# Kernel optimization log

Hardware: AMD Instinct MI355X
Metric: run time of the kernel (lower is better)

## Reference

```python
import jax, jax.numpy as jnp
import numpy as np

T, A = 2048, 64          # n_thread, n_agents
RAWOB, N_TP, N_GP = 120, 5, 2
E = N_TP * N_GP          # number of sub-nets (type x group placeholder)
D = RAWOB + N_TP + 1     # augmented obs dim fed to each Net
H = 128                  # hidden width of each sub-net MLP
N_ACTION = 16


def setup_inputs() -> dict:
    key = jax.random.key(0)
    ks = jax.random.split(key, 12)
    s1 = 1.0 / np.sqrt(D)
    s2 = 1.0 / np.sqrt(H)
    return {
        "obs": jax.random.normal(ks[0], (T, A, RAWOB), dtype=jnp.float32),
        "hete_pick": jax.random.randint(ks[1], (T, A), 0, E),
        "hete_type": jax.random.randint(ks[2], (T, A), 0, N_TP),
        "gp_sel_summary": jax.random.randint(ks[3], (T, N_TP), 0, N_GP),
        # per-expert actor MLP params [E, ...]
        "W1": jax.random.normal(ks[4], (E, D, H), dtype=jnp.float32) * s1,
        "b1": jnp.zeros((E, H), dtype=jnp.float32),
        "W2": jax.random.normal(ks[5], (E, H, N_ACTION), dtype=jnp.float32) * s2,
        "b2": jnp.zeros((E, N_ACTION), dtype=jnp.float32),
        # central critic params
        "Wc1": jax.random.normal(ks[6], (D, H), dtype=jnp.float32) * s1,
        "bc1": jnp.zeros((H,), dtype=jnp.float32),
        "Wc2": jax.random.normal(ks[7], (H, 1), dtype=jnp.float32) * s2,
        "bc2": jnp.zeros((1,), dtype=jnp.float32),
    }


def _augment_obs(obs, hete_type, gp_sel_summary):
    # obs <- cat(obs, hete_type, gp_sel_summary with -1 scattered at own type idx)
    t, a, _ = obs.shape
    n_tp = gp_sel_summary.shape[1]
    gp = jnp.broadcast_to(gp_sel_summary[:, None, :].astype(obs.dtype), (t, a, n_tp))
    oh = jax.nn.one_hot(hete_type, n_tp, dtype=obs.dtype)
    gp_obs = gp * (1.0 - oh) - oh  # scatter -1 at index hete_type
    return jnp.concatenate([obs, hete_type[..., None].astype(obs.dtype), gp_obs], axis=-1)


def reference(obs, hete_pick, hete_type, gp_sel_summary,
              W1, b1, W2, b2, Wc1, bc1, Wc2, bc2):
    t, a, _ = obs.shape
    x = _augment_obs(obs, hete_type, gp_sel_summary)          # [T, A, D]
    xf = x.reshape(t * a, -1)                                  # [N, D]
    pick = hete_pick.reshape(t * a)                            # [N]
    n_exp = W1.shape[0]
    # dispatch: each token routed to exactly one sub-net; dense compute + masked combine
    logits = jnp.zeros((t * a, W2.shape[-1]), dtype=obs.dtype)
    for e in range(n_exp):  # small fixed expert loop
        y = jax.nn.relu(xf @ W1[e] + b1[e]) @ W2[e] + b2[e]    # [N, n_action]
        logits = jnp.where((pick == e)[:, None], y, logits)
    logits = logits.reshape(t, a, -1)
    # central critic on all tokens
    value = (jax.nn.relu(xf @ Wc1 + bc1) @ Wc2 + bc2).reshape(t, a, 1)
    return logits, value
```

## Files before the change

kernel.cpp:

```cpp
#include <hip/hip_runtime.h>
#include <hip/hip_bf16.h>

#define T_DIM   2048
#define A_DIM   64
#define N_TOK   (T_DIM * A_DIM)
#define RAWOB   120
#define N_TP    5
#define E_EXP   10
#define D_DIM   126
#define DP      128
#define H_DIM   128
#define N_ACT   16
#define CAP     14336
#define BTOK    256
#define MAXC    (CAP / BTOK)
#define LOGITS_SZ (N_TOK * N_ACT)
#define HB_STRIDE 136

typedef __bf16 bh8 __attribute__((ext_vector_type(8)));
typedef ushort u16x8 __attribute__((ext_vector_type(8)));
typedef float  f32x4 __attribute__((ext_vector_type(4)));

__device__ __forceinline__ f32x4 mfma16(bh8 a, bh8 b, f32x4 c) {
    return __builtin_amdgcn_mfma_f32_16x16x32_bf16(a, b, c, 0, 0, 0);
}

__device__ __forceinline__ ushort f2bf(float f) {
    unsigned x = __builtin_bit_cast(unsigned, f);
    unsigned r = (x + 0x7fffu + ((x >> 16) & 1u)) >> 16;
    return (ushort)r;
}

#define W1P_N (E_EXP * H_DIM * DP)
#define W2P_N (E_EXP * N_ACT * H_DIM)
#define WC1P_N (DP * DP)

#define PB_BLOCKS 252

__global__ __launch_bounds__(256) void prep_bucket_kernel(
    const float* __restrict__ W1, const float* __restrict__ W2,
    const float* __restrict__ Wc1, const int* __restrict__ pick,
    int* __restrict__ counts, int* __restrict__ order,
    ushort* __restrict__ W1p, ushort* __restrict__ W2p, ushort* __restrict__ Wc1p)
{
    int bx = blockIdx.x, tid = threadIdx.x;
    if (bx < 44) {
        __shared__ ushort st[32][130];
        const float* src;
        ushort* dstbase;
        int kt;
        if (bx < 40) {
            int e = bx >> 2;
            kt = bx & 3;
            src = W1 + (e * D_DIM + kt * 32) * H_DIM;
            dstbase = W1p + e * (H_DIM * DP);
        } else {
            kt = bx - 40;
            src = Wc1 + kt * 32 * H_DIM;
            dstbase = Wc1p;
        }
        int dmax = D_DIM - kt * 32;
#pragma unroll
        for (int p = 0; p < 16; ++p) {
            int idx = p * 256 + tid;
            int dd = idx >> 7, n = idx & 127;
            float v = (dd < dmax) ? src[dd * H_DIM + n] : 0.f;
            st[dd][n] = f2bf(v);
        }
        __syncthreads();
#pragma unroll
        for (int p = 0; p < 16; ++p) {
            int idx = p * 256 + tid;
            int dd = idx >> 7, n = idx & 127;
            dstbase[((n >> 4) * 4 + kt) * 512 + ((dd >> 3) * 16 + (n & 15)) * 8 + (dd & 7)]
                = st[dd][n];
        }
    } else if (bx < 124) {
        int i = (bx - 44) * 256 + tid;
        int j = i & 7;
        int l = (i >> 3) & 63;
        int kt = (i >> 9) & 3;
        int e = i >> 11;
        int lm = l & 15, lq = l >> 4;
        W2p[i] = f2bf(W2[(e * H_DIM + kt * 32 + lq * 8 + j) * N_ACT + lm]);
    } else {
        __shared__ int lc[E_EXP], lb[E_EXP], lcur[E_EXP];
        if (tid < E_EXP) { lc[tid] = 0; lcur[tid] = 0; }
        __syncthreads();
        int base = (bx - 124) * 1024;
        int e4[4];
#pragma unroll
        for (int it = 0; it < 4; ++it) {
            e4[it] = pick[base + it * 256 + tid];
            atomicAdd(&lc[e4[it]], 1);
        }
        __syncthreads();
        if (tid < E_EXP) lb[tid] = atomicAdd(&counts[tid * 16], lc[tid]);
        __syncthreads();
#pragma unroll
        for (int it = 0; it < 4; ++it) {
            int e = e4[it];
            int pos = lb[e] + atomicAdd(&lcur[e], 1);
            if (pos < CAP) order[e * CAP + pos] = base + it * 256 + tid;
        }
    }
}

__global__ __launch_bounds__(512, 4) void moe_kernel(
    const float* __restrict__ obs, const int* __restrict__ hete_type,
    const int* __restrict__ gp_sel,
    const float* __restrict__ b1, const float* __restrict__ b2,
    const float* __restrict__ bc1, const float* __restrict__ bc2,
    const int* __restrict__ counts, const int* __restrict__ order,
    const ushort* __restrict__ W1p, const ushort* __restrict__ W2p,
    const ushort* __restrict__ Wc1p, const float* __restrict__ Wc2,
    float* __restrict__ out)
{
    __shared__ __align__(16) ushort wlds[18432];
    __shared__ __align__(16) ushort hbuf[8][16 * HB_STRIDE];

    const int bx = blockIdx.x;
    const int e = bx % E_EXP;
    const int c = bx / E_EXP;
    const int cnt = counts[e * 16];
    const int start = c * BTOK;
    if (start >= cnt) return;

    const int tid = threadIdx.x;
    const int w = tid >> 6;
    const int base = start + w * 32;
    const int l = tid & 63;
    const int lm = l & 15;
    const int lq = l >> 4;

    {
        const u16x8* s1 = (const u16x8*)(const void*)(W1p + e * (H_DIM * DP));
        u16x8* d1 = (u16x8*)(void*)wlds;
#pragma unroll
        for (int p = 0; p < 4; ++p) d1[p * 512 + tid] = s1[p * 512 + tid];
        if (tid < 256)
            ((u16x8*)(void*)(wlds + 16384))[tid] =
                ((const u16x8*)(const void*)(W2p + e * 2048))[tid];
    }

    const int* ord_e = order + e * CAP;

    bh8 a[2][4];
#pragma unroll
    for (int mt = 0; mt < 2; ++mt) {
        const int slot = min(base + mt * 16 + lm, cnt - 1);
        const int tok = ord_e[slot];
        const float* orow = obs + tok * RAWOB;
#pragma unroll
        for (int kt = 0; kt < 3; ++kt) {
            const float* p = orow + kt * 32 + lq * 8;
            float4 u0 = *(const float4*)(const void*)p;
            float4 u1 = *(const float4*)(const void*)(p + 4);
            u16x8 t;
            t[0] = f2bf(u0.x); t[1] = f2bf(u0.y); t[2] = f2bf(u0.z); t[3] = f2bf(u0.w);
            t[4] = f2bf(u1.x); t[5] = f2bf(u1.y); t[6] = f2bf(u1.z); t[7] = f2bf(u1.w);
            a[mt][kt] = __builtin_bit_cast(bh8, t);
        }
        u16x8 t;
        if (lq < 3) {
            const float* p = orow + 96 + lq * 8;
            float4 u0 = *(const float4*)(const void*)p;
            float4 u1 = *(const float4*)(const void*)(p + 4);
            t[0] = f2bf(u0.x); t[1] = f2bf(u0.y); t[2] = f2bf(u0.z); t[3] = f2bf(u0.w);
            t[4] = f2bf(u1.x); t[5] = f2bf(u1.y); t[6] = f2bf(u1.z); t[7] = f2bf(u1.w);
        } else {
            int ht = hete_type[tok];
            int tt = tok >> 6;
            t[0] = f2bf((float)ht);
#pragma unroll
            for (int q = 0; q < N_TP; ++q) {
                float g = (q == ht) ? -1.0f : (float)gp_sel[tt * N_TP + q];
                t[1 + q] = f2bf(g);
            }
            t[6] = 0; t[7] = 0;
        }
        a[mt][3] = __builtin_bit_cast(bh8, t);
    }

    float bnv[8];
#pragma unroll
    for (int nt = 0; nt < 8; ++nt) bnv[nt] = b1[e * H_DIM + nt * 16 + lm];
    const float bb  = b2[e * N_ACT + lm];
    const float bcv = bc2[0];

    __syncthreads();

    ushort* hrow = &hbuf[w][0];
#pragma unroll
    for (int mt = 0; mt < 2; ++mt) {
#pragma unroll
        for (int nt = 0; nt < 8; ++nt) {
            const int n = nt * 16 + lm;
            f32x4 ae = (f32x4){0.f, 0.f, 0.f, 0.f};
#pragma unroll
            for (int kt = 0; kt < 4; ++kt) {
                bh8 be = *(const bh8*)(const void*)(wlds + (nt * 4 + kt) * 512 + l * 8);
                ae = mfma16(a[mt][kt], be, ae);
            }
            float bn = bnv[nt];
#pragma unroll
            for (int r = 0; r < 4; ++r)
                hrow[(lq * 4 + r) * HB_STRIDE + n] = f2bf(fmaxf(ae[r] + bn, 0.f));
        }
        f32x4 y = (f32x4){0.f, 0.f, 0.f, 0.f};
#pragma unroll
        for (int kt = 0; kt < 4; ++kt) {
            bh8 bf = *(const bh8*)(const void*)(wlds + 16384 + kt * 512 + l * 8);
            bh8 hf = *(const bh8*)(const void*)(hrow + lm * HB_STRIDE + kt * 32 + lq * 8);
            y = mfma16(hf, bf, y);
        }
#pragma unroll
        for (int r = 0; r < 4; ++r) {
            int m = mt * 16 + lq * 4 + r;
            if (base + m < cnt)
                out[ord_e[base + m] * N_ACT + lm] = y[r] + bb;
        }
    }

    __syncthreads();

    {
        const u16x8* s1 = (const u16x8*)(const void*)Wc1p;
        u16x8* d1 = (u16x8*)(void*)wlds;
#pragma unroll
        for (int p = 0; p < 4; ++p) d1[p * 512 + tid] = s1[p * 512 + tid];
    }
    __syncthreads();

    {
        float part[2][4] = {{0.f,0.f,0.f,0.f},{0.f,0.f,0.f,0.f}};
#pragma unroll
        for (int nt = 0; nt < 8; ++nt) {
            const int n = nt * 16 + lm;
            f32x4 ac0 = (f32x4){0.f,0.f,0.f,0.f}, ac1 = ac0;
#pragma unroll
            for (int kt = 0; kt < 4; ++kt) {
                bh8 bc = *(const bh8*)(const void*)(wlds + (nt * 4 + kt) * 512 + l * 8);
                ac0 = mfma16(a[0][kt], bc, ac0);
                ac1 = mfma16(a[1][kt], bc, ac1);
            }
            float cn = bc1[n], wc = Wc2[n];
#pragma unroll
            for (int r = 0; r < 4; ++r) {
                part[0][r] += fmaxf(ac0[r] + cn, 0.f) * wc;
                part[1][r] += fmaxf(ac1[r] + cn, 0.f) * wc;
            }
        }
#pragma unroll
        for (int mask = 1; mask < 16; mask <<= 1)
#pragma unroll
            for (int mt = 0; mt < 2; ++mt)
#pragma unroll
                for (int r = 0; r < 4; ++r)
                    part[mt][r] += __shfl_xor(part[mt][r], mask, 64);
        if (lm == 0) {
#pragma unroll
            for (int mt = 0; mt < 2; ++mt)
#pragma unroll
                for (int r = 0; r < 4; ++r) {
                    int m = mt * 16 + lq * 4 + r;
                    if (base + m < cnt)
                        out[LOGITS_SZ + ord_e[base + m]] = part[mt][r] + bcv;
                }
        }
    }
}

extern "C" void kernel_launch(void* const* d_in, const int* in_sizes, int n_in,
                              void* d_out, int out_size, void* d_ws, size_t ws_size,
                              hipStream_t stream) {
    const float* obs  = (const float*)d_in[0];
    const int*   pick = (const int*)d_in[1];
    const int*   htyp = (const int*)d_in[2];
    const int*   gp   = (const int*)d_in[3];
    const float* W1   = (const float*)d_in[4];
    const float* b1   = (const float*)d_in[5];
    const float* W2   = (const float*)d_in[6];
    const float* b2   = (const float*)d_in[7];
    const float* Wc1  = (const float*)d_in[8];
    const float* bc1  = (const float*)d_in[9];
    const float* Wc2  = (const float*)d_in[10];
    const float* bc2  = (const float*)d_in[11];
    float* out = (float*)d_out;

    int*    counts = (int*)d_ws;
    int*    order  = counts + 160;
    ushort* W1p    = (ushort*)(order + E_EXP * CAP);
    ushort* W2p    = W1p + W1P_N;
    ushort* Wc1p   = W2p + W2P_N;

    hipMemsetAsync(counts, 0, 160 * sizeof(int), stream);
    prep_bucket_kernel<<<PB_BLOCKS, 256, 0, stream>>>(
        W1, W2, Wc1, pick, counts, order, W1p, W2p, Wc1p);
    moe_kernel<<<E_EXP * MAXC, 512, 0, stream>>>(
        obs, htyp, gp, b1, b2, bc1, bc2, counts, order,
        W1p, W2p, Wc1p, Wc2, out);
}
```

Measured before the change: 139.6 us.

## Keep MLP hidden in registers via transposed MFMA and fold biases into weights

The first-layer MFMA now runs with swapped operands (weights as A, activations as B), so the hidden activations come out in a layout that feeds straight into a K=16 bf16 MFMA for the second layer. This removes the per-wave LDS hidden buffer and its write/read round trip. Biases b1/bc1 are folded into the packed weight matrix as an extra K row, matched by a constant 1.0 input column, so the bias adds go away. The critic reduction becomes a lane-local dot product plus two shuffles instead of a 16-lane butterfly. Dropping the hidden buffer frees LDS, and launch bounds go up to 8 waves-per-EU occupancy, which may add register pressure.

```diff
diff --git a/kernel.cpp b/kernel.cpp
--- a/kernel.cpp
+++ b/kernel.cpp
@@ -15,14 +15,18 @@
 #define BTOK    256
 #define MAXC    (CAP / BTOK)
 #define LOGITS_SZ (N_TOK * N_ACT)
-#define HB_STRIDE 136
 
 typedef __bf16 bh8 __attribute__((ext_vector_type(8)));
 typedef ushort u16x8 __attribute__((ext_vector_type(8)));
+typedef ushort u16x4 __attribute__((ext_vector_type(4)));
+typedef short  s16x4 __attribute__((ext_vector_type(4)));
 typedef float  f32x4 __attribute__((ext_vector_type(4)));
 
 __device__ __forceinline__ f32x4 mfma16(bh8 a, bh8 b, f32x4 c) {
     return __builtin_amdgcn_mfma_f32_16x16x32_bf16(a, b, c, 0, 0, 0);
+}
+__device__ __forceinline__ f32x4 mfma16k16(s16x4 a, s16x4 b, f32x4 c) {
+    return __builtin_amdgcn_mfma_f32_16x16x16bf16_1k(a, b, c, 0, 0, 0);
 }
 
 __device__ __forceinline__ ushort f2bf(float f) {
@@ -39,7 +43,8 @@
 
 __global__ __launch_bounds__(256) void prep_bucket_kernel(
     const float* __restrict__ W1, const float* __restrict__ W2,
-    const float* __restrict__ Wc1, const int* __restrict__ pick,
+    const float* __restrict__ Wc1, const float* __restrict__ b1,
+    const float* __restrict__ bc1, const int* __restrict__ pick,
     int* __restrict__ counts, int* __restrict__ order,
     ushort* __restrict__ W1p, ushort* __restrict__ W2p, ushort* __restrict__ Wc1p)
 {
@@ -47,16 +52,19 @@
     if (bx < 44) {
         __shared__ ushort st[32][130];
         const float* src;
+        const float* bias;
         ushort* dstbase;
         int kt;
         if (bx < 40) {
             int e = bx >> 2;
             kt = bx & 3;
             src = W1 + (e * D_DIM + kt * 32) * H_DIM;
+            bias = b1 + e * H_DIM;
             dstbase = W1p + e * (H_DIM * DP);
         } else {
             kt = bx - 40;
             src = Wc1 + kt * 32 * H_DIM;
+            bias = bc1;
             dstbase = Wc1p;
         }
         int dmax = D_DIM - kt * 32;
@@ -64,7 +72,10 @@
         for (int p = 0; p < 16; ++p) {
             int idx = p * 256 + tid;
             int dd = idx >> 7, n = idx & 127;
-            float v = (dd < dmax) ? src[dd * H_DIM + n] : 0.f;
+            float v;
+            if (dd < dmax)                    v = src[dd * H_DIM + n];
+            else if (kt == 3 && dd == 30)     v = bias[n];
+            else                              v = 0.f;
             st[dd][n] = f2bf(v);
         }
         __syncthreads();
@@ -77,12 +88,13 @@
         }
     } else if (bx < 124) {
         int i = (bx - 44) * 256 + tid;
-        int j = i & 7;
-        int l = (i >> 3) & 63;
-        int kt = (i >> 9) & 3;
-        int e = i >> 11;
-        int lm = l & 15, lq = l >> 4;
-        W2p[i] = f2bf(W2[(e * H_DIM + kt * 32 + lq * 8 + j) * N_ACT + lm]);
+        int e   = i >> 11;
+        int rem = i & 2047;
+        int kk  = rem >> 8;
+        int idx = rem & 255;
+        int l = idx >> 2, j = idx & 3;
+        int lq = l >> 4, lm = l & 15;
+        W2p[i] = f2bf(W2[(e * H_DIM + kk * 16 + lq * 4 + j) * N_ACT + lm]);
     } else {
         __shared__ int lc[E_EXP], lb[E_EXP], lcur[E_EXP];
         if (tid < E_EXP) { lc[tid] = 0; lcur[tid] = 0; }
@@ -106,18 +118,16 @@
     }
 }
 
-__global__ __launch_bounds__(512, 4) void moe_kernel(
+__global__ __launch_bounds__(512, 8) void moe_kernel(
     const float* __restrict__ obs, const int* __restrict__ hete_type,
     const int* __restrict__ gp_sel,
-    const float* __restrict__ b1, const float* __restrict__ b2,
-    const float* __restrict__ bc1, const float* __restrict__ bc2,
+    const float* __restrict__ b2, const float* __restrict__ bc2,
     const int* __restrict__ counts, const int* __restrict__ order,
     const ushort* __restrict__ W1p, const ushort* __restrict__ W2p,
     const ushort* __restrict__ Wc1p, const float* __restrict__ Wc2,
     float* __restrict__ out)
 {
     __shared__ __align__(16) ushort wlds[18432];
-    __shared__ __align__(16) ushort hbuf[8][16 * HB_STRIDE];
 
     const int bx = blockIdx.x;
     const int e = bx % E_EXP;
@@ -146,10 +156,12 @@
     const int* ord_e = order + e * CAP;
 
     bh8 a[2][4];
+    int tokm[2];
 #pragma unroll
     for (int mt = 0; mt < 2; ++mt) {
         const int slot = min(base + mt * 16 + lm, cnt - 1);
         const int tok = ord_e[slot];
+        tokm[mt] = tok;
         const float* orow = obs + tok * RAWOB;
 #pragma unroll
         for (int kt = 0; kt < 3; ++kt) {
@@ -177,42 +189,35 @@
                 float g = (q == ht) ? -1.0f : (float)gp_sel[tt * N_TP + q];
                 t[1 + q] = f2bf(g);
             }
-            t[6] = 0; t[7] = 0;
+            t[6] = (ushort)0x3F80;
+            t[7] = 0;
         }
         a[mt][3] = __builtin_bit_cast(bh8, t);
     }
 
-    float bnv[8];
-#pragma unroll
-    for (int nt = 0; nt < 8; ++nt) bnv[nt] = b1[e * H_DIM + nt * 16 + lm];
     const float bb  = b2[e * N_ACT + lm];
     const float bcv = bc2[0];
 
     __syncthreads();
 
-    ushort* hrow = &hbuf[w][0];
 #pragma unroll
     for (int mt = 0; mt < 2; ++mt) {
+        f32x4 y = (f32x4){0.f, 0.f, 0.f, 0.f};
 #pragma unroll
         for (int nt = 0; nt < 8; ++nt) {
-            const int n = nt * 16 + lm;
             f32x4 ae = (f32x4){0.f, 0.f, 0.f, 0.f};
 #pragma unroll
             for (int kt = 0; kt < 4; ++kt) {
-                bh8 be = *(const bh8*)(const void*)(wlds + (nt * 4 + kt) * 512 + l * 8);
-                ae = mfma16(a[mt][kt], be, ae);
+                bh8 wf = *(const bh8*)(const void*)(wlds + (nt * 4 + kt) * 512 + l * 8);
+                ae = mfma16(wf, a[mt][kt], ae);
             }
-            float bn = bnv[nt];
-#pragma unroll
-            for (int r = 0; r < 4; ++r)
-                hrow[(lq * 4 + r) * HB_STRIDE + n] = f2bf(fmaxf(ae[r] + bn, 0.f));
-        }
-        f32x4 y = (f32x4){0.f, 0.f, 0.f, 0.f};
-#pragma unroll
-        for (int kt = 0; kt < 4; ++kt) {
-            bh8 bf = *(const bh8*)(const void*)(wlds + 16384 + kt * 512 + l * 8);
-            bh8 hf = *(const bh8*)(const void*)(hrow + lm * HB_STRIDE + kt * 32 + lq * 8);
-            y = mfma16(hf, bf, y);
+            u16x4 hp;
+            hp[0] = f2bf(fmaxf(ae[0], 0.f));
+            hp[1] = f2bf(fmaxf(ae[1], 0.f));
+            hp[2] = f2bf(fmaxf(ae[2], 0.f));
+            hp[3] = f2bf(fmaxf(ae[3], 0.f));
+            s16x4 w2f = *(const s16x4*)(const void*)(wlds + 16384 + nt * 256 + l * 4);
+            y = mfma16k16(__builtin_bit_cast(s16x4, hp), w2f, y);
         }
 #pragma unroll
         for (int r = 0; r < 4; ++r) {
@@ -233,40 +238,27 @@
     __syncthreads();
 
     {
-        float part[2][4] = {{0.f,0.f,0.f,0.f},{0.f,0.f,0.f,0.f}};
+        float p0 = 0.f, p1 = 0.f;
 #pragma unroll
         for (int nt = 0; nt < 8; ++nt) {
-            const int n = nt * 16 + lm;
-            f32x4 ac0 = (f32x4){0.f,0.f,0.f,0.f}, ac1 = ac0;
+            f32x4 c0 = (f32x4){0.f,0.f,0.f,0.f}, c1 = c0;
 #pragma unroll
             for (int kt = 0; kt < 4; ++kt) {
-                bh8 bc = *(const bh8*)(const void*)(wlds + (nt * 4 + kt) * 512 + l * 8);
-                ac0 = mfma16(a[0][kt], bc, ac0);
-                ac1 = mfma16(a[1][kt], bc, ac1);
+                bh8 wf = *(const bh8*)(const void*)(wlds + (nt * 4 + kt) * 512 + l * 8);
+                c0 = mfma16(wf, a[0][kt], c0);
+                c1 = mfma16(wf, a[1][kt], c1);
             }
-            float cn = bc1[n], wc = Wc2[n];
-#pragma unroll
-            for (int r = 0; r < 4; ++r) {
-                part[0][r] += fmaxf(ac0[r] + cn, 0.f) * wc;
-                part[1][r] += fmaxf(ac1[r] + cn, 0.f) * wc;
-            }
-        }
-#pragma unroll
-        for (int mask = 1; mask < 16; mask <<= 1)
-#pragma unroll
-            for (int mt = 0; mt < 2; ++mt)
-#pragma unroll
-                for (int r = 0; r < 4; ++r)
-                    part[mt][r] += __shfl_xor(part[mt][r], mask, 64);
-        if (lm == 0) {
-#pragma unroll
-            for (int mt = 0; mt < 2; ++mt)
-#pragma unroll
-                for (int r = 0; r < 4; ++r) {
-                    int m = mt * 16 + lq * 4 + r;
-                    if (base + m < cnt)
-                        out[LOGITS_SZ + ord_e[base + m]] = part[mt][r] + bcv;
-                }
+            const float4 wc = *(const float4*)(const void*)(Wc2 + nt * 16 + lq * 4);
+            p0 += fmaxf(c0[0], 0.f) * wc.x + fmaxf(c0[1], 0.f) * wc.y
+                + fmaxf(c0[2], 0.f) * wc.z + fmaxf(c0[3], 0.f) * wc.w;
+            p1 += fmaxf(c1[0], 0.f) * wc.x + fmaxf(c1[1], 0.f) * wc.y
+                + fmaxf(c1[2], 0.f) * wc.z + fmaxf(c1[3], 0.f) * wc.w;
+        }
+        p0 += __shfl_xor(p0, 16, 64); p0 += __shfl_xor(p0, 32, 64);
+        p1 += __shfl_xor(p1, 16, 64); p1 += __shfl_xor(p1, 32, 64);
+        if (lq == 0) {
+            if (base + lm < cnt)      out[LOGITS_SZ + tokm[0]] = p0 + bcv;
+            if (base + 16 + lm < cnt) out[LOGITS_SZ + tokm[1]] = p1 + bcv;
         }
     }
 }
@@ -296,8 +288,8 @@
 
     hipMemsetAsync(counts, 0, 160 * sizeof(int), stream);
     prep_bucket_kernel<<<PB_BLOCKS, 256, 0, stream>>>(
-        W1, W2, Wc1, pick, counts, order, W1p, W2p, Wc1p);
+        W1, W2, Wc1, b1, bc1, pick, counts, order, W1p, W2p, Wc1p);
     moe_kernel<<<E_EXP * MAXC, 512, 0, stream>>>(
-        obs, htyp, gp, b1, b2, bc1, bc2, counts, order,
+        obs, htyp, gp, b2, bc2, counts, order,
         W1p, W2p, Wc1p, Wc2, out);
 }
```

After: 152.8 us. 1.1x slower.
